# Kernel tuning notes

Hardware: AMD Instinct MI355X
Metric: run time of the kernel (lower is better)

## Reference

```python
import jax, jax.numpy as jnp
import numpy as np

N_NODES = 50000
NEG_SLOPE = 0.2
EPS = 1e-16


def _gat_conv(x, src, dst, W, a_src, a_dst, bias, heads, out_c, concat):
    """PyG-style GATConv (self-loops assumed already added to src/dst)."""
    N = x.shape[0]
    h = (x @ W).reshape(N, heads, out_c)                 # [N,H,C]
    s_src = jnp.sum(h * a_src, axis=-1)                  # [N,H]
    s_dst = jnp.sum(h * a_dst, axis=-1)                  # [N,H]
    e = jax.nn.leaky_relu(s_src[src] + s_dst[dst], NEG_SLOPE)  # [E,H]
    # segment softmax over incoming edges of each dst node
    m = jax.ops.segment_max(e, dst, num_segments=N)      # [N,H]
    e = jnp.exp(e - m[dst])
    z = jax.ops.segment_sum(e, dst, num_segments=N)      # [N,H]
    alpha = e / (z[dst] + EPS)                           # [E,H]
    out = jax.ops.segment_sum(h[src] * alpha[:, :, None], dst, num_segments=N)  # [N,H,C]
    if concat:
        out = out.reshape(N, heads * out_c)
    else:
        out = out.mean(axis=1)
    return out + bias


def setup_inputs() -> dict:
    key = jax.random.key(0)
    ks = jax.random.split(key, 12)
    N, E, nfeat, nhid, nclass = N_NODES, 800000, 512, 256, 40
    heads, head_dim = 4, nhid // 4
    g = lambda k, shape, fan: (jax.random.normal(k, shape, jnp.float32) * (1.0 / np.sqrt(fan)))
    return {
        "x": jax.random.normal(ks[0], (N, nfeat), jnp.float32),
        "adj": jax.random.randint(ks[1], (2, E), 0, N, jnp.int64),
        "W1": g(ks[2], (nfeat, heads * head_dim), nfeat),
        "att_src1": g(ks[3], (heads, head_dim), head_dim),
        "att_dst1": g(ks[4], (heads, head_dim), head_dim),
        "b1": jnp.zeros((heads * head_dim,), jnp.float32),
        "W2": g(ks[5], (nhid, nclass), nhid),
        "att_src2": g(ks[6], (1, nclass), nclass),
        "att_dst2": g(ks[7], (1, nclass), nclass),
        "b2": jnp.zeros((nclass,), jnp.float32),
    }


def reference(x, adj, W1, att_src1, att_dst1, b1, W2, att_src2, att_dst2, b2):
    N = x.shape[0]
    loops = jnp.arange(N, dtype=adj.dtype)
    src = jnp.concatenate([adj[0], loops])   # PyG GATConv add_self_loops=True
    dst = jnp.concatenate([adj[1], loops])
    h = _gat_conv(x, src, dst, W1, att_src1, att_dst1, b1, heads=4, out_c=64, concat=True)
    h = jax.nn.relu(h)
    # dropout: eval mode => identity
    out = _gat_conv(h, src, dst, W2, att_src2, att_dst2, b2, heads=1, out_c=40, concat=False)
    return out
```

## Files before the change

kernel.cpp:

```cpp
#include <hip/hip_runtime.h>
#include <hip/hip_bf16.h>
#include <math.h>

#define NFEAT 512
#define NHID 256
#define HEADS 4
#define HDIM 64
#define NCLASS 40
#define NEG_SLOPE 0.2f
#define EPS_Z 1e-16f

typedef short bf16x8 __attribute__((ext_vector_type(8)));
typedef float f32x4 __attribute__((ext_vector_type(4)));

__device__ __forceinline__ float lrelu(float x) {
  return x > 0.f ? x : NEG_SLOPE * x;
}

__device__ __forceinline__ ushort f2bf(float f) {
  union { float f; uint u; } c; c.f = f;
  uint u = c.u;
  uint r = u + 0x7FFFu + ((u >> 16) & 1u);
  return (ushort)(r >> 16);
}
__device__ __forceinline__ float bf2f(ushort h) {
  union { uint u; float f; } c; c.u = ((uint)h) << 16;
  return c.f;
}

__device__ __forceinline__ uint cvtpk(float lo, float hi) {
  uint r;
  asm("v_cvt_pk_bf16_f32 %0, %1, %2" : "=v"(r) : "v"(lo), "v"(hi));
  return r;
}


__global__ void count_kernel(const int* __restrict__ dstv, int E, int* __restrict__ counts) {
  int i = blockIdx.x * blockDim.x + threadIdx.x;
  if (i < E) atomicAdd(&counts[dstv[i]], 1);
}

__global__ __launch_bounds__(1024) void scan_a(const int* __restrict__ counts,
    int* __restrict__ excl, int* __restrict__ bsum, int n) {
  __shared__ int tmp[1024];
  int t = threadIdx.x;
  int i = blockIdx.x * 1024 + t;
  int v = (i < n) ? counts[i] : 0;
  tmp[t] = v;
  __syncthreads();
  for (int off = 1; off < 1024; off <<= 1) {
    int u = (t >= off) ? tmp[t - off] : 0;
    __syncthreads();
    tmp[t] += u;
    __syncthreads();
  }
  if (i < n) excl[i] = tmp[t] - v;
  if (t == 1023) bsum[blockIdx.x] = tmp[t];
}

__global__ __launch_bounds__(1024) void scan_b(int* __restrict__ bsum, int nb) {
  __shared__ int tmp[1024];
  int t = threadIdx.x;
  tmp[t] = (t < nb) ? bsum[t] : 0;
  __syncthreads();
  for (int off = 1; off < 1024; off <<= 1) {
    int u = (t >= off) ? tmp[t - off] : 0;
    __syncthreads();
    tmp[t] += u;
    __syncthreads();
  }
  if (t < nb) bsum[t] = tmp[t];
}

__global__ void scan_c(const int* __restrict__ excl, const int* __restrict__ bsum_incl,
    int* __restrict__ row_off, int* __restrict__ cursor, int n, int E) {
  int i = blockIdx.x * blockDim.x + threadIdx.x;
  if (i < n) {
    int b = i >> 10;
    int off = (b > 0) ? bsum_incl[b - 1] : 0;
    int v = excl[i] + off;
    row_off[i] = v;
    cursor[i] = v;
  }
  if (i == 0) row_off[n] = E;
}

__global__ void scatter_kernel(const int* __restrict__ srcv, const int* __restrict__ dstv,
                               int E, int* __restrict__ cursor, int* __restrict__ edge_src) {
  int i = blockIdx.x * blockDim.x + threadIdx.x;
  if (i < E) {
    int pos = atomicAdd(&cursor[dstv[i]], 1);
    edge_src[pos] = srcv[i];
  }
}


__global__ __launch_bounds__(64) void wprep_kernel(const float* __restrict__ W,
    ushort* __restrict__ Bh) {
  int fb = blockIdx.x;
  int ct = fb >> 4, ks = fb & 15;
  int l = threadIdx.x;
  int g = l >> 4, rr = l & 15;
  uint hw[4];
  #pragma unroll
  for (int p = 0; p < 4; ++p) {
    ushort h2v[2];
    #pragma unroll
    for (int q = 0; q < 2; ++q) {
      int e = p * 2 + q;
      int k = ks * 32 + 4 * g + (e & 3) + 16 * (e >> 2);
      int col = ct * 16 + rr;
      h2v[q] = f2bf(W[k * NHID + col]);
    }
    hw[p] = (uint)h2v[0] | ((uint)h2v[1] << 16);
  }
  size_t o = ((size_t)fb * 64 + l) * 8;
  uint4 hv; hv.x = hw[0]; hv.y = hw[1]; hv.z = hw[2]; hv.w = hw[3];
  *(uint4*)&Bh[o] = hv;
}


__global__ __launch_bounds__(256, 4) void gemm1_mfma(const float* __restrict__ A,
    const ushort* __restrict__ Bh,
    const float* __restrict__ asrc, const float* __restrict__ adst,
    ushort* __restrict__ h1b, float* __restrict__ ssrc1, float* __restrict__ sdst1,
    int M) {
  __shared__ float A_s[2][64 * 64];
  const int tid = threadIdx.x;
  const int lane = tid & 63;
  const int wc = tid >> 6;
  const int g = lane >> 4, rr = lane & 15;
  const int row0 = blockIdx.x * 64;

  f32x4 acc[4][4] = {};

  auto stage = [&](int ki, int buf) {
    #pragma unroll
    for (int j = 0; j < 4; ++j) {
      int grp = wc * 4 + j;
      int s = grp * 64 + lane;
      int r = s >> 4;
      int us = s & 15;
      int ud = us ^ (r & 7);
      int gr = row0 + r;
      if (gr >= M) gr = M - 1;
      const float* src = &A[(size_t)gr * NFEAT + ki * 64 + ud * 4];
      float* dst = &A_s[buf][grp * 256];
      __builtin_amdgcn_global_load_lds(
          (const __attribute__((address_space(1))) float*)src,
          (__attribute__((address_space(3))) float*)dst, 16, 0, 0);
    }
  };

  stage(0, 0);
  __syncthreads();

  for (int ki = 0; ki < 8; ++ki) {
    const int cur = ki & 1;
    if (ki < 7) stage(ki + 1, cur ^ 1);

    #pragma unroll
    for (int kk = 0; kk < 2; ++kk) {
      const int ks = ki * 2 + kk;
      bf16x8 bhf[4];
      #pragma unroll
      for (int ni = 0; ni < 4; ++ni) {
        int ct = wc * 4 + ni;
        size_t bidx = ((size_t)(ct * 16 + ks) * 64 + lane) * 8;
        bhf[ni] = *(const bf16x8*)&Bh[bidx];
      }
      #pragma unroll
      for (int mi = 0; mi < 4; ++mi) {
        int row = mi * 16 + rr;
        int u0 = (8 * kk + g) ^ (row & 7);
        int u1 = (8 * kk + 4 + g) ^ (row & 7);
        f32x4 lo = *(const f32x4*)&A_s[cur][row * 64 + u0 * 4];
        f32x4 hi = *(const f32x4*)&A_s[cur][row * 64 + u1 * 4];
        uint w0 = cvtpk(lo[0], lo[1]);
        uint w1 = cvtpk(lo[2], lo[3]);
        uint w2 = cvtpk(hi[0], hi[1]);
        uint w3 = cvtpk(hi[2], hi[3]);
        union { uint u[4]; bf16x8 v; } af;
        af.u[0] = w0; af.u[1] = w1; af.u[2] = w2; af.u[3] = w3;
        #pragma unroll
        for (int ni = 0; ni < 4; ++ni) {
          acc[mi][ni] = __builtin_amdgcn_mfma_f32_16x16x32_bf16(af.v, bhf[ni], acc[mi][ni], 0, 0, 0);
        }
      }
    }
    __syncthreads();
  }

  float a_s[4], a_d[4];
  #pragma unroll
  for (int ni = 0; ni < 4; ++ni) {
    a_s[ni] = asrc[wc * 64 + ni * 16 + rr];
    a_d[ni] = adst[wc * 64 + ni * 16 + rr];
  }

  #pragma unroll
  for (int mi = 0; mi < 4; ++mi) {
    #pragma unroll
    for (int j = 0; j < 4; ++j) {
      int r = row0 + mi * 16 + g * 4 + j;
      bool ok = r < M;
      float ps = 0.f, pd = 0.f;
      #pragma unroll
      for (int ni = 0; ni < 4; ++ni) {
        float v = acc[mi][ni][j];
        ps += v * a_s[ni];
        pd += v * a_d[ni];
        if (ok) h1b[(size_t)r * NHID + wc * 64 + ni * 16 + rr] = f2bf(v);
      }
      #pragma unroll
      for (int m = 1; m < 16; m <<= 1) {
        ps += __shfl_xor(ps, m, 64);
        pd += __shfl_xor(pd, m, 64);
      }
      if (ok && rr == 0) {
        ssrc1[r * HEADS + wc] = ps;
        sdst1[r * HEADS + wc] = pd;
      }
    }
  }
}


__global__ __launch_bounds__(256) void gemm2_fused(const float* __restrict__ A,
    const float* __restrict__ B, const float* __restrict__ asrc,
    const float* __restrict__ adst, ushort* __restrict__ h2b,
    float* __restrict__ ssrc2, float* __restrict__ sdst2, int M) {
  __shared__ float As[16][64 + 1];
  __shared__ float Bs[16][68];
  const int tid = threadIdx.x;
  const int tx = tid & 15, ty = tid >> 4;
  const int row0 = blockIdx.x * 64;
  float acc[4][4] = {};

  const int la_r = tid >> 2;
  const int la_k = (tid & 3) * 4;
  const int lb_r = tid >> 4;
  const int lb_c = (tid & 15) * 4;

  for (int k0 = 0; k0 < NHID; k0 += 16) {
    float4 av = make_float4(0.f, 0.f, 0.f, 0.f);
    int ar = row0 + la_r;
    if (ar < M) av = *(const float4*)&A[(size_t)ar * NHID + k0 + la_k];
    As[la_k + 0][la_r] = av.x;
    As[la_k + 1][la_r] = av.y;
    As[la_k + 2][la_r] = av.z;
    As[la_k + 3][la_r] = av.w;

    float4 bv = make_float4(0.f, 0.f, 0.f, 0.f);
    const float* Brow = &B[(size_t)(k0 + lb_r) * NCLASS];
    if (lb_c + 3 < NCLASS) bv = *(const float4*)&Brow[lb_c];
    *(float4*)&Bs[lb_r][lb_c] = bv;
    __syncthreads();

    #pragma unroll
    for (int k = 0; k < 16; ++k) {
      float a0 = As[k][ty * 4 + 0];
      float a1 = As[k][ty * 4 + 1];
      float a2 = As[k][ty * 4 + 2];
      float a3 = As[k][ty * 4 + 3];
      float4 b = *(const float4*)&Bs[k][tx * 4];
      acc[0][0] += a0 * b.x; acc[0][1] += a0 * b.y; acc[0][2] += a0 * b.z; acc[0][3] += a0 * b.w;
      acc[1][0] += a1 * b.x; acc[1][1] += a1 * b.y; acc[1][2] += a1 * b.z; acc[1][3] += a1 * b.w;
      acc[2][0] += a2 * b.x; acc[2][1] += a2 * b.y; acc[2][2] += a2 * b.z; acc[2][3] += a2 * b.w;
      acc[3][0] += a3 * b.x; acc[3][1] += a3 * b.y; acc[3][2] += a3 * b.z; acc[3][3] += a3 * b.w;
    }
    __syncthreads();
  }

  const int cbase = tx * 4;
  const bool cok = cbase + 3 < NCLASS;
  float4 av_s = make_float4(0.f, 0.f, 0.f, 0.f);
  float4 av_d = make_float4(0.f, 0.f, 0.f, 0.f);
  if (cok) {
    av_s = *(const float4*)&asrc[cbase];
    av_d = *(const float4*)&adst[cbase];
  }

  #pragma unroll
  for (int i = 0; i < 4; ++i) {
    int r = row0 + ty * 4 + i;
    bool ok = r < M;
    float ps = acc[i][0] * av_s.x + acc[i][1] * av_s.y + acc[i][2] * av_s.z + acc[i][3] * av_s.w;
    float pd = acc[i][0] * av_d.x + acc[i][1] * av_d.y + acc[i][2] * av_d.z + acc[i][3] * av_d.w;
    #pragma unroll
    for (int m = 1; m < 16; m <<= 1) {
      ps += __shfl_xor(ps, m, 64);
      pd += __shfl_xor(pd, m, 64);
    }
    if (ok && cok) {
      ushort4 o;
      o.x = f2bf(acc[i][0]); o.y = f2bf(acc[i][1]);
      o.z = f2bf(acc[i][2]); o.w = f2bf(acc[i][3]);
      *(ushort4*)&h2b[(size_t)r * NCLASS + cbase] = o;
    }
    if (ok && tx == 0) { ssrc2[r] = ps; sdst2[r] = pd; }
  }
}


__global__ __launch_bounds__(64) void agg1_kernel(const ushort* __restrict__ h1b,
    const float* __restrict__ s_src, const float* __restrict__ s_dst,
    const int* __restrict__ row_off, const int* __restrict__ edge_src,
    const float* __restrict__ b1, float* __restrict__ hrelu) {
  int v = blockIdx.x;
  int l = threadIdx.x;
  int head = l >> 4;
  int c = l * 4;
  float sdv = s_dst[v * HEADS + head];

  float w = __expf(lrelu(s_src[v * HEADS + head] + sdv));
  ushort4 hv = *(const ushort4*)&h1b[(size_t)v * NHID + c];
  float4 acc = make_float4(w * bf2f(hv.x), w * bf2f(hv.y), w * bf2f(hv.z), w * bf2f(hv.w));
  float z = w;

  int i = row_off[v], end = row_off[v + 1];
  int u_next = (i < end) ? edge_src[i] : 0;
  for (; i < end; ++i) {
    int u = u_next;
    if (i + 1 < end) u_next = edge_src[i + 1];
    float wu = __expf(lrelu(s_src[u * HEADS + head] + sdv));
    ushort4 hu = *(const ushort4*)&h1b[(size_t)u * NHID + c];
    acc.x += wu * bf2f(hu.x);
    acc.y += wu * bf2f(hu.y);
    acc.z += wu * bf2f(hu.z);
    acc.w += wu * bf2f(hu.w);
    z += wu;
  }
  float inv = 1.f / (z + EPS_Z);
  float4 bb = *(const float4*)&b1[c];
  float4 o;
  o.x = fmaxf(acc.x * inv + bb.x, 0.f);
  o.y = fmaxf(acc.y * inv + bb.y, 0.f);
  o.z = fmaxf(acc.z * inv + bb.z, 0.f);
  o.w = fmaxf(acc.w * inv + bb.w, 0.f);
  *(float4*)&hrelu[(size_t)v * NHID + c] = o;
}

__global__ __launch_bounds__(64) void agg2_kernel(const ushort* __restrict__ h2b,
    const float* __restrict__ s_src, const float* __restrict__ s_dst,
    const int* __restrict__ row_off, const int* __restrict__ edge_src,
    const float* __restrict__ b2, float* __restrict__ out) {
  int v = blockIdx.x;
  int l = threadIdx.x;
  bool act = l < NCLASS;
  float sdv = s_dst[v];

  float w = __expf(lrelu(s_src[v] + sdv));
  float acc = act ? w * bf2f(h2b[(size_t)v * NCLASS + l]) : 0.f;
  float z = w;

  int i = row_off[v], end = row_off[v + 1];
  int u_next = (i < end) ? edge_src[i] : 0;
  for (; i < end; ++i) {
    int u = u_next;
    if (i + 1 < end) u_next = edge_src[i + 1];
    float wu = __expf(lrelu(s_src[u] + sdv));
    if (act) acc += wu * bf2f(h2b[(size_t)u * NCLASS + l]);
    z += wu;
  }
  if (act) out[(size_t)v * NCLASS + l] = acc / (z + EPS_Z) + b2[l];
}


extern "C" void kernel_launch(void* const* d_in, const int* in_sizes, int n_in,
                              void* d_out, int out_size, void* d_ws, size_t ws_size,
                              hipStream_t stream) {
  const float* x   = (const float*)d_in[0];
  const int*   adj = (const int*)d_in[1];
  const float* W1  = (const float*)d_in[2];
  const float* as1 = (const float*)d_in[3];
  const float* ad1 = (const float*)d_in[4];
  const float* b1  = (const float*)d_in[5];
  const float* W2  = (const float*)d_in[6];
  const float* as2 = (const float*)d_in[7];
  const float* ad2 = (const float*)d_in[8];
  const float* b2  = (const float*)d_in[9];
  float* out = (float*)d_out;

  const int N = in_sizes[0] / NFEAT;
  const int E = in_sizes[1] / 2;

  char* ws = (char*)d_ws;
  size_t off = 0;
  auto alloc = [&](size_t bytes) -> void* {
    void* p = ws + off;
    off = (off + bytes + 255) & ~(size_t)255;
    return p;
  };
  ushort* h1b   = (ushort*)alloc((size_t)N * NHID * 2);
  float* hrelu  = (float*)alloc((size_t)N * NHID * 4);
  ushort* h2b   = (ushort*)alloc((size_t)N * NCLASS * 2);
  float* ssrc1  = (float*)alloc((size_t)N * HEADS * 4);
  float* sdst1  = (float*)alloc((size_t)N * HEADS * 4);
  float* ssrc2  = (float*)alloc((size_t)N * 4);
  float* sdst2  = (float*)alloc((size_t)N * 4);
  int* counts   = (int*)alloc((size_t)N * 4);
  int* cursor   = (int*)alloc((size_t)N * 4);
  int* row_off  = (int*)alloc((size_t)(N + 1) * 4);
  int* edge_src = (int*)alloc((size_t)E * 4);
  int* excl     = (int*)alloc((size_t)N * 4);
  int* bsum     = (int*)alloc((size_t)1024 * 4);
  ushort* whp   = (ushort*)alloc((size_t)NFEAT * NHID * 2);
  (void)ws_size;

  const int* srcv = adj;
  const int* dstv = adj + E;
  const int nb = (N + 1023) / 1024;

  wprep_kernel<<<256, 64, 0, stream>>>(W1, whp);

  hipMemsetAsync(counts, 0, (size_t)N * 4, stream);
  count_kernel<<<(E + 255) / 256, 256, 0, stream>>>(dstv, E, counts);
  scan_a<<<nb, 1024, 0, stream>>>(counts, excl, bsum, N);
  scan_b<<<1, 1024, 0, stream>>>(bsum, nb);
  scan_c<<<(N + 255) / 256, 256, 0, stream>>>(excl, bsum, row_off, cursor, N, E);
  scatter_kernel<<<(E + 255) / 256, 256, 0, stream>>>(srcv, dstv, E, cursor, edge_src);

  gemm1_mfma<<<(N + 63) / 64, 256, 0, stream>>>(x, whp, as1, ad1, h1b, ssrc1, sdst1, N);
  agg1_kernel<<<N, 64, 0, stream>>>(h1b, ssrc1, sdst1, row_off, edge_src, b1, hrelu);

  gemm2_fused<<<(N + 63) / 64, 256, 0, stream>>>(hrelu, W2, as2, ad2, h2b, ssrc2, sdst2, N);
  agg2_kernel<<<N, 64, 0, stream>>>(h2b, ssrc2, sdst2, row_off, edge_src, b2, out);
}
```

Measured before the change: 306.1 us.

## Precompute layer-1 edge weights, store hidden activations as bf16, pack aggregation blocks

Result: slower. 354.3 us (+15.8%).

```diff
diff --git a/kernel.cpp b/kernel.cpp
--- a/kernel.cpp
+++ b/kernel.cpp
@@ -86,11 +86,31 @@
 }
 
 __global__ void scatter_kernel(const int* __restrict__ srcv, const int* __restrict__ dstv,
-                               int E, int* __restrict__ cursor, int* __restrict__ edge_src) {
+                               int E, int* __restrict__ cursor,
+                               int* __restrict__ edge_src, int* __restrict__ edge_dst) {
   int i = blockIdx.x * blockDim.x + threadIdx.x;
   if (i < E) {
-    int pos = atomicAdd(&cursor[dstv[i]], 1);
+    int d = dstv[i];
+    int pos = atomicAdd(&cursor[d], 1);
     edge_src[pos] = srcv[i];
+    edge_dst[pos] = d;
+  }
+}
+
+__global__ void ew_kernel(const int* __restrict__ edge_src, const int* __restrict__ edge_dst,
+                          const float* __restrict__ ssrc1, const float* __restrict__ sdst1,
+                          float4* __restrict__ ew, int E) {
+  int i = blockIdx.x * blockDim.x + threadIdx.x;
+  if (i < E) {
+    int u = edge_src[i], v = edge_dst[i];
+    float4 a = *(const float4*)&ssrc1[u * HEADS];
+    float4 b = *(const float4*)&sdst1[v * HEADS];
+    float4 w;
+    w.x = __expf(lrelu(a.x + b.x));
+    w.y = __expf(lrelu(a.y + b.y));
+    w.z = __expf(lrelu(a.z + b.z));
+    w.w = __expf(lrelu(a.w + b.w));
+    ew[i] = w;
   }
 }
 
@@ -226,7 +246,7 @@
 }
 
 
-__global__ __launch_bounds__(256) void gemm2_fused(const float* __restrict__ A,
+__global__ __launch_bounds__(256) void gemm2_fused(const ushort* __restrict__ A,
     const float* __restrict__ B, const float* __restrict__ asrc,
     const float* __restrict__ adst, ushort* __restrict__ h2b,
     float* __restrict__ ssrc2, float* __restrict__ sdst2, int M) {
@@ -243,13 +263,16 @@
   const int lb_c = (tid & 15) * 4;
 
   for (int k0 = 0; k0 < NHID; k0 += 16) {
-    float4 av = make_float4(0.f, 0.f, 0.f, 0.f);
+    float a0 = 0.f, a1 = 0.f, a2 = 0.f, a3 = 0.f;
     int ar = row0 + la_r;
-    if (ar < M) av = *(const float4*)&A[(size_t)ar * NHID + k0 + la_k];
-    As[la_k + 0][la_r] = av.x;
-    As[la_k + 1][la_r] = av.y;
-    As[la_k + 2][la_r] = av.z;
-    As[la_k + 3][la_r] = av.w;
+    if (ar < M) {
+      ushort4 uv = *(const ushort4*)&A[(size_t)ar * NHID + k0 + la_k];
+      a0 = bf2f(uv.x); a1 = bf2f(uv.y); a2 = bf2f(uv.z); a3 = bf2f(uv.w);
+    }
+    As[la_k + 0][la_r] = a0;
+    As[la_k + 1][la_r] = a1;
+    As[la_k + 2][la_r] = a2;
+    As[la_k + 3][la_r] = a3;
 
     float4 bv = make_float4(0.f, 0.f, 0.f, 0.f);
     const float* Brow = &B[(size_t)(k0 + lb_r) * NCLASS];
@@ -259,15 +282,15 @@
 
     #pragma unroll
     for (int k = 0; k < 16; ++k) {
-      float a0 = As[k][ty * 4 + 0];
-      float a1 = As[k][ty * 4 + 1];
-      float a2 = As[k][ty * 4 + 2];
-      float a3 = As[k][ty * 4 + 3];
+      float x0 = As[k][ty * 4 + 0];
+      float x1 = As[k][ty * 4 + 1];
+      float x2 = As[k][ty * 4 + 2];
+      float x3 = As[k][ty * 4 + 3];
       float4 b = *(const float4*)&Bs[k][tx * 4];
-      acc[0][0] += a0 * b.x; acc[0][1] += a0 * b.y; acc[0][2] += a0 * b.z; acc[0][3] += a0 * b.w;
-      acc[1][0] += a1 * b.x; acc[1][1] += a1 * b.y; acc[1][2] += a1 * b.z; acc[1][3] += a1 * b.w;
-      acc[2][0] += a2 * b.x; acc[2][1] += a2 * b.y; acc[2][2] += a2 * b.z; acc[2][3] += a2 * b.w;
-      acc[3][0] += a3 * b.x; acc[3][1] += a3 * b.y; acc[3][2] += a3 * b.z; acc[3][3] += a3 * b.w;
+      acc[0][0] += x0 * b.x; acc[0][1] += x0 * b.y; acc[0][2] += x0 * b.z; acc[0][3] += x0 * b.w;
+      acc[1][0] += x1 * b.x; acc[1][1] += x1 * b.y; acc[1][2] += x1 * b.z; acc[1][3] += x1 * b.w;
+      acc[2][0] += x2 * b.x; acc[2][1] += x2 * b.y; acc[2][2] += x2 * b.z; acc[2][3] += x2 * b.w;
+      acc[3][0] += x3 * b.x; acc[3][1] += x3 * b.y; acc[3][2] += x3 * b.z; acc[3][3] += x3 * b.w;
     }
     __syncthreads();
   }
@@ -303,50 +326,60 @@
 }
 
 
-__global__ __launch_bounds__(64) void agg1_kernel(const ushort* __restrict__ h1b,
+__global__ __launch_bounds__(256) void agg1_kernel(const ushort* __restrict__ h1b,
     const float* __restrict__ s_src, const float* __restrict__ s_dst,
     const int* __restrict__ row_off, const int* __restrict__ edge_src,
-    const float* __restrict__ b1, float* __restrict__ hrelu) {
-  int v = blockIdx.x;
-  int l = threadIdx.x;
+    const float* __restrict__ ewf, const float* __restrict__ b1,
+    ushort* __restrict__ hrelu_b, int n) {
+  int v = blockIdx.x * 4 + (threadIdx.x >> 6);
+  if (v >= n) return;
+  int l = threadIdx.x & 63;
   int head = l >> 4;
   int c = l * 4;
-  float sdv = s_dst[v * HEADS + head];
-
-  float w = __expf(lrelu(s_src[v * HEADS + head] + sdv));
+
+  float w = __expf(lrelu(s_src[v * HEADS + head] + s_dst[v * HEADS + head]));
   ushort4 hv = *(const ushort4*)&h1b[(size_t)v * NHID + c];
   float4 acc = make_float4(w * bf2f(hv.x), w * bf2f(hv.y), w * bf2f(hv.z), w * bf2f(hv.w));
   float z = w;
 
   int i = row_off[v], end = row_off[v + 1];
-  int u_next = (i < end) ? edge_src[i] : 0;
+  int u_n = 0; float w_n = 0.f; ushort4 r_n = make_ushort4(0, 0, 0, 0);
+  if (i < end) {
+    u_n = edge_src[i];
+    w_n = ewf[(size_t)i * HEADS + head];
+    r_n = *(const ushort4*)&h1b[(size_t)u_n * NHID + c];
+  }
   for (; i < end; ++i) {
-    int u = u_next;
-    if (i + 1 < end) u_next = edge_src[i + 1];
-    float wu = __expf(lrelu(s_src[u * HEADS + head] + sdv));
-    ushort4 hu = *(const ushort4*)&h1b[(size_t)u * NHID + c];
-    acc.x += wu * bf2f(hu.x);
-    acc.y += wu * bf2f(hu.y);
-    acc.z += wu * bf2f(hu.z);
-    acc.w += wu * bf2f(hu.w);
+    float wu = w_n;
+    ushort4 ru = r_n;
+    if (i + 1 < end) {
+      u_n = edge_src[i + 1];
+      w_n = ewf[(size_t)(i + 1) * HEADS + head];
+      r_n = *(const ushort4*)&h1b[(size_t)u_n * NHID + c];
+    }
+    acc.x += wu * bf2f(ru.x);
+    acc.y += wu * bf2f(ru.y);
+    acc.z += wu * bf2f(ru.z);
+    acc.w += wu * bf2f(ru.w);
     z += wu;
   }
   float inv = 1.f / (z + EPS_Z);
   float4 bb = *(const float4*)&b1[c];
-  float4 o;
-  o.x = fmaxf(acc.x * inv + bb.x, 0.f);
-  o.y = fmaxf(acc.y * inv + bb.y, 0.f);
-  o.z = fmaxf(acc.z * inv + bb.z, 0.f);
-  o.w = fmaxf(acc.w * inv + bb.w, 0.f);
-  *(float4*)&hrelu[(size_t)v * NHID + c] = o;
-}
-
-__global__ __launch_bounds__(64) void agg2_kernel(const ushort* __restrict__ h2b,
+  ushort4 o;
+  o.x = f2bf(fmaxf(acc.x * inv + bb.x, 0.f));
+  o.y = f2bf(fmaxf(acc.y * inv + bb.y, 0.f));
+  o.z = f2bf(fmaxf(acc.z * inv + bb.z, 0.f));
+  o.w = f2bf(fmaxf(acc.w * inv + bb.w, 0.f));
+  *(ushort4*)&hrelu_b[(size_t)v * NHID + c] = o;
+}
+
+__global__ __launch_bounds__(256) void agg2_kernel(const ushort* __restrict__ h2b,
     const float* __restrict__ s_src, const float* __restrict__ s_dst,
     const int* __restrict__ row_off, const int* __restrict__ edge_src,
-    const float* __restrict__ b2, float* __restrict__ out) {
-  int v = blockIdx.x;
-  int l = threadIdx.x;
+    const float* __restrict__ b2, float* __restrict__ out, int n) {
+  int v = blockIdx.x * 4 + (threadIdx.x >> 6);
+  if (v >= n) return;
+  int l = threadIdx.x & 63;
   bool act = l < NCLASS;
   float sdv = s_dst[v];
 
@@ -392,20 +425,22 @@
     off = (off + bytes + 255) & ~(size_t)255;
     return p;
   };
-  ushort* h1b   = (ushort*)alloc((size_t)N * NHID * 2);
-  float* hrelu  = (float*)alloc((size_t)N * NHID * 4);
-  ushort* h2b   = (ushort*)alloc((size_t)N * NCLASS * 2);
-  float* ssrc1  = (float*)alloc((size_t)N * HEADS * 4);
-  float* sdst1  = (float*)alloc((size_t)N * HEADS * 4);
-  float* ssrc2  = (float*)alloc((size_t)N * 4);
-  float* sdst2  = (float*)alloc((size_t)N * 4);
-  int* counts   = (int*)alloc((size_t)N * 4);
-  int* cursor   = (int*)alloc((size_t)N * 4);
-  int* row_off  = (int*)alloc((size_t)(N + 1) * 4);
-  int* edge_src = (int*)alloc((size_t)E * 4);
-  int* excl     = (int*)alloc((size_t)N * 4);
-  int* bsum     = (int*)alloc((size_t)1024 * 4);
-  ushort* whp   = (ushort*)alloc((size_t)NFEAT * NHID * 2);
+  ushort* h1b    = (ushort*)alloc((size_t)N * NHID * 2);
+  ushort* hrelub = (ushort*)alloc((size_t)N * NHID * 2);
+  ushort* h2b    = (ushort*)alloc((size_t)N * NCLASS * 2);
+  float* ssrc1   = (float*)alloc((size_t)N * HEADS * 4);
+  float* sdst1   = (float*)alloc((size_t)N * HEADS * 4);
+  float* ssrc2   = (float*)alloc((size_t)N * 4);
+  float* sdst2   = (float*)alloc((size_t)N * 4);
+  int* counts    = (int*)alloc((size_t)N * 4);
+  int* cursor    = (int*)alloc((size_t)N * 4);
+  int* row_off   = (int*)alloc((size_t)(N + 1) * 4);
+  int* edge_src  = (int*)alloc((size_t)E * 4);
+  int* edge_dst  = (int*)alloc((size_t)E * 4);
+  float4* ew     = (float4*)alloc((size_t)E * 16);
+  int* excl      = (int*)alloc((size_t)N * 4);
+  int* bsum      = (int*)alloc((size_t)1024 * 4);
+  ushort* whp    = (ushort*)alloc((size_t)NFEAT * NHID * 2);
   (void)ws_size;
 
   const int* srcv = adj;
@@ -419,11 +454,13 @@
   scan_a<<<nb, 1024, 0, stream>>>(counts, excl, bsum, N);
   scan_b<<<1, 1024, 0, stream>>>(bsum, nb);
   scan_c<<<(N + 255) / 256, 256, 0, stream>>>(excl, bsum, row_off, cursor, N, E);
-  scatter_kernel<<<(E + 255) / 256, 256, 0, stream>>>(srcv, dstv, E, cursor, edge_src);
+  scatter_kernel<<<(E + 255) / 256, 256, 0, stream>>>(srcv, dstv, E, cursor, edge_src, edge_dst);
 
   gemm1_mfma<<<(N + 63) / 64, 256, 0, stream>>>(x, whp, as1, ad1, h1b, ssrc1, sdst1, N);
-  agg1_kernel<<<N, 64, 0, stream>>>(h1b, ssrc1, sdst1, row_off, edge_src, b1, hrelu);
-
-  gemm2_fused<<<(N + 63) / 64, 256, 0, stream>>>(hrelu, W2, as2, ad2, h2b, ssrc2, sdst2, N);
-  agg2_kernel<<<N, 64, 0, stream>>>(h2b, ssrc2, sdst2, row_off, edge_src, b2, out);
-}
+  ew_kernel<<<(E + 255) / 256, 256, 0, stream>>>(edge_src, edge_dst, ssrc1, sdst1, ew, E);
+  agg1_kernel<<<(N + 3) / 4, 256, 0, stream>>>(h1b, ssrc1, sdst1, row_off, edge_src,
+                                               (const float*)ew, b1, hrelub, N);
+
+  gemm2_fused<<<(N + 63) / 64, 256, 0, stream>>>(hrelub, W2, as2, ad2, h2b, ssrc2, sdst2, N);
+  agg2_kernel<<<(N + 3) / 4, 256, 0, stream>>>(h2b, ssrc2, sdst2, row_off, edge_src, b2, out, N);
+}
```
